# Optimization experiments

Measured on AMD Instinct MI355X. Metric: run time of the kernel, lower is better.

Reference implementation:

```python
import jax, jax.numpy as jnp
import numpy as np

B, INP, OUP = 16, 64, 64
T, H, W = 30, 64, 44
KD, KH, KW = 3, 3, 3
M, G = 2, 2
INP_GAP = max(16, INP // 16)          # 16
GROUPS = G * OUP                       # 128 (wn_fc2 groups)
IN_PG = (M * OUP) // GROUPS            # 1  in-channels per group
OUT_PG = (OUP * INP * KD * KH * KW) // GROUPS  # 864 out-channels per group


def setup_inputs() -> dict:
    key = jax.random.key(0)
    ks = jax.random.split(key, 6)
    x = jax.random.normal(ks[0], (B, INP, T, H, W), dtype=jnp.float32)
    # reduce: 1x1x1 conv INP -> INP_GAP (with bias), acts on [B, INP, 1,1,1]
    w_reduce = jax.random.normal(ks[1], (INP_GAP, INP), dtype=jnp.float32) * 0.05
    b_reduce = jax.random.normal(ks[2], (INP_GAP,), dtype=jnp.float32) * 0.05
    # wn_fc1: 1x1x1 conv INP_GAP -> M*OUP (with bias)
    w_fc1 = jax.random.normal(ks[3], (M * OUP, INP_GAP), dtype=jnp.float32) * 0.05
    b_fc1 = jax.random.normal(ks[4], (M * OUP,), dtype=jnp.float32) * 0.05
    # wn_fc2: grouped 1x1x1 conv, no bias: [groups, out_per_group, in_per_group]
    w_fc2 = jax.random.normal(ks[5], (GROUPS, OUT_PG, IN_PG), dtype=jnp.float32) * 0.02
    return {"x": x, "w_reduce": w_reduce, "b_reduce": b_reduce,
            "w_fc1": w_fc1, "b_fc1": b_fc1, "w_fc2": w_fc2}


def reference(x, w_reduce, b_reduce, w_fc1, b_fc1, w_fc2):
    # Global average pool over T,H,W -> [B, INP]; 1x1x1 convs are matmuls.
    x_gap = x.mean(axis=(2, 3, 4))                       # [B, INP]
    g = x_gap @ w_reduce.T + b_reduce                     # [B, INP_GAP]
    h = jax.nn.sigmoid(g @ w_fc1.T + b_fc1)               # [B, M*OUP]
    # Grouped 1x1 conv (groups=GROUPS): group-major channel layout matches
    # torch's conv output ordering, so a plain reshape reproduces .view().
    hg = h.reshape(B, GROUPS, IN_PG)                      # [B, G*OUP, 1]
    wdyn = jnp.einsum('goi,bgi->bgo', w_fc2, hg)          # [B, GROUPS, OUT_PG]
    wdyn = wdyn.reshape(B, OUP, INP, KD, KH, KW)          # per-sample conv weights

    # Per-sample conv3d (groups=1), stride 1, padding 1 on D,H,W.
    def conv_one(xi, wi):
        # xi: [INP, T, H, W], wi: [OUP, INP, KD, KH, KW]
        return jax.lax.conv_general_dilated(
            xi[None], wi, window_strides=(1, 1, 1),
            padding=[(1, 1), (1, 1), (1, 1)],
            dimension_numbers=('NCDHW', 'OIDHW', 'NCDHW'))[0]

    return jax.vmap(conv_one)(x, wdyn)                    # [B, OUP, T, H, W]
```

## Files before the change

kernel.cpp:

```cpp
#include <hip/hip_runtime.h>
#include <hip/hip_bf16.h>
#include <stdint.h>

#define B_ 16
#define T_ 30
#define H_ 64
#define W_ 44
#define HW_ (H_*W_)
#define THW_ (T_*HW_)

#define HP_ 66
#define WP_ 46
#define PPLANE_ (HP_*WP_)
#define PPOS_ (T_*PPLANE_)

#define TZ 4
#define TY 8
#define TX 16
#define SZ 6
#define SY 10
#define SX 18
#define NS (SZ*SY*SX)

typedef __bf16 bf16x8 __attribute__((ext_vector_type(8)));
typedef float f32x4 __attribute__((ext_vector_type(4)));

static __device__ __forceinline__ short f2bf(float f) {
    __hip_bfloat16 h = __float2bfloat16(f);
    union { __hip_bfloat16 b; short s; } u; u.b = h; return u.s;
}

static __device__ __forceinline__ void gload_lds16(const short* g, short* l) {
    __builtin_amdgcn_global_load_lds((const __attribute__((address_space(1))) void*)g,
                                     (__attribute__((address_space(3))) void*)l, 16, 0, 0);
}

__global__ __launch_bounds__(256) void transpose_kernel(const float* __restrict__ x,
                                                        short* __restrict__ xt) {
    __shared__ short lb[64*52];
    int blk = blockIdx.x;
    int b = blk / (T_*HP_);
    int r = blk - b*(T_*HP_);
    int t = r / HP_;
    int hp = r - t*HP_;
    int tid = threadIdx.x;
    bool interior = (hp >= 1) && (hp <= H_);
    if (interior) {
        int h = hp - 1;
        for (int e = tid; e < 704; e += 256) {
            int ic = e / 11, q = e - ic*11;
            const float4* p = (const float4*)(x + ((size_t)(b*64 + ic)*T_ + t)*HW_ + h*W_) + q;
            float4 v = *p;
            short4 s4;
            s4.x = f2bf(v.x); s4.y = f2bf(v.y); s4.z = f2bf(v.z); s4.w = f2bf(v.w);
            *(short4*)&lb[ic*52 + q*4] = s4;
        }
    }
    __syncthreads();
    for (int e = tid; e < WP_*16; e += 256) {
        int wp = e >> 4, i4 = (e & 15) * 4;
        short4 s4 = make_short4(0,0,0,0);
        if (interior && wp >= 1 && wp <= W_) {
            int w = wp - 1;
            s4.x = lb[(i4+0)*52 + w];
            s4.y = lb[(i4+1)*52 + w];
            s4.z = lb[(i4+2)*52 + w];
            s4.w = lb[(i4+3)*52 + w];
        }
        size_t pos = (size_t)t*PPLANE_ + hp*WP_ + wp;
        short* dst = xt + ((size_t)(b*2 + (i4 >> 5))*PPOS_ + pos)*32 + (i4 & 31);
        *(short4*)dst = s4;
    }
}

__global__ __launch_bounds__(256) void gap_kernel(const float* __restrict__ x,
                                                  float* __restrict__ gap) {
    int bc = blockIdx.x;
    const float4* p4 = (const float4*)(x + (size_t)bc * THW_);
    float sum = 0.f;
    for (int i = threadIdx.x; i < THW_ / 4; i += 256) {
        float4 v = p4[i];
        sum += (v.x + v.y) + (v.z + v.w);
    }
    #pragma unroll
    for (int o = 32; o > 0; o >>= 1) sum += __shfl_down(sum, o);
    __shared__ float partial[4];
    if ((threadIdx.x & 63) == 0) partial[threadIdx.x >> 6] = sum;
    __syncthreads();
    if (threadIdx.x == 0)
        gap[bc] = (partial[0] + partial[1] + partial[2] + partial[3]) * (1.0f / THW_);
}

__global__ __launch_bounds__(256) void fc_kernel(const float* __restrict__ gap,
        const float* __restrict__ w_reduce, const float* __restrict__ b_reduce,
        const float* __restrict__ w_fc1, const float* __restrict__ b_fc1,
        float* __restrict__ h_out) {
    __shared__ float gl[256];
    int t = threadIdx.x;
    {
        int b = t >> 4, j = t & 15;
        float a = b_reduce[j];
        #pragma unroll
        for (int c = 0; c < 64; ++c) a += gap[b*64 + c] * w_reduce[j*64 + c];
        gl[b*16 + j] = a;
    }
    __syncthreads();
    for (int idx = t; idx < 2048; idx += 256) {
        int b = idx >> 7, j = idx & 127;
        float v = b_fc1[j];
        #pragma unroll
        for (int i = 0; i < 16; ++i) v += gl[b*16 + i] * w_fc1[j*16 + i];
        h_out[idx] = 1.0f / (1.0f + expf(-v));
    }
}

__global__ __launch_bounds__(256) void wdyn_kernel(const float* __restrict__ w_fc2,
        const float* __restrict__ h, short* __restrict__ wdyn, short* __restrict__ zblk) {
    if (blockIdx.x == 0 && threadIdx.x < 128) zblk[threadIdx.x] = 0;
    int b = blockIdx.x / 27, tap = blockIdx.x % 27;
    short* dst = wdyn + ((size_t)b*27 + tap) * 4096;
    for (int e = threadIdx.x; e < 4096; e += 256) {
        int oc = e >> 6, ic = e & 63;
        float wv = w_fc2[(oc*64 + ic)*27 + tap];
        float hv = h[b*128 + 2*oc + (ic >> 5)];
        dst[e] = f2bf(wv * hv);
    }
}

__global__ __launch_bounds__(256, 2) void conv_kernel(const short* __restrict__ xt,
        const short* __restrict__ wdyn, const short* __restrict__ zblk,
        float* __restrict__ out) {
    __shared__ short xs[NS*32 + 256];
    __shared__ short wb[2][2048];

    int bid = blockIdx.x;
    int b = bid / 192; int r = bid - b*192;
    int tzt = r / 24; r -= tzt*24;
    int tyt = r / 3;  int txt = r - tyt*3;
    int t0 = tzt*TZ, h0 = tyt*TY, w0 = txt*TX;

    int tid = threadIdx.x, wid = tid >> 6, lane = tid & 63;
    int ln = lane & 15, kg = lane >> 4;
    int l4 = lane >> 2, c = lane & 3;

    const short* wdb = wdyn + (size_t)b * 27 * 4096;

    f32x4 acc[4][8];
    #pragma unroll
    for (int mt = 0; mt < 4; ++mt)
        #pragma unroll
        for (int j = 0; j < 8; ++j) acc[mt][j] = f32x4{0.f, 0.f, 0.f, 0.f};

    auto stage_w = [&](int step) {
        int tap = step % 27, half = step / 27;
        const short* base = wdb + tap*4096 + half*32;
        short* dst = wb[step & 1];
        #pragma unroll
        for (int jj = 0; jj < 4; ++jj) {
            int oc = jj*16 + l4;
            gload_lds16(base + oc*64 + ((c ^ (oc & 3)) * 8), dst + jj*512);
        }
    };
    auto stage_x = [&](int half) {
        const short* xbh = xt + (size_t)(b*2 + half) * PPOS_ * 32;
        #pragma unroll 2
        for (int ii = 0; ii < 17; ++ii) {
            int inst = wid*17 + ii;
            int s = inst*16 + l4;
            int z = s / 180; int rr = s - z*180;
            int y = rr / 18; int xx = rr - y*18;
            int t = t0 + z - 1;
            int seg = (c ^ (s & 3)) * 8;
            const short* src = ((unsigned)t < (unsigned)T_)
                ? xbh + ((size_t)t*PPLANE_ + (h0+y)*WP_ + (w0+xx))*32 + seg
                : zblk + seg;
            gload_lds16(src, xs + inst*512);
        }
    };

    stage_x(0);
    if (wid == 0) stage_w(0);
    __syncthreads();

    for (int step = 0; step < 54; ++step) {
        int nstep = step + 1;
        if (nstep < 54 && wid == (nstep & 3)) stage_w(nstep);

        int tap = step % 27;
        int kd = tap / 9; int rr = tap - kd*9; int kh = rr / 3; int kw = rr - kh*3;
        const short* wbp = wb[step & 1];
        bf16x8 a[4];
        #pragma unroll
        for (int mt = 0; mt < 4; ++mt) {
            int oc = mt*16 + ln;
            a[mt] = *(const bf16x8*)&wbp[oc*32 + ((kg ^ (oc & 3)) * 8)];
        }
        int sb = (wid + kd)*180 + kh*18 + kw + ln;
        #pragma unroll
        for (int j = 0; j < 8; ++j) {
            int s = sb + j*18;
            bf16x8 bv = *(const bf16x8*)&xs[s*32 + ((kg ^ (s & 3)) * 8)];
            acc[0][j] = __builtin_amdgcn_mfma_f32_16x16x32_bf16(a[0], bv, acc[0][j], 0, 0, 0);
            acc[1][j] = __builtin_amdgcn_mfma_f32_16x16x32_bf16(a[1], bv, acc[1][j], 0, 0, 0);
            acc[2][j] = __builtin_amdgcn_mfma_f32_16x16x32_bf16(a[2], bv, acc[2][j], 0, 0, 0);
            acc[3][j] = __builtin_amdgcn_mfma_f32_16x16x32_bf16(a[3], bv, acc[3][j], 0, 0, 0);
        }
        __syncthreads();
        if (step == 26) { stage_x(1); __syncthreads(); }
    }

    int t = t0 + wid;
    int wv = w0 + ln;
    if (t < T_ && wv < W_) {
        #pragma unroll
        for (int mt = 0; mt < 4; ++mt) {
            size_t obase = ((size_t)(b*64 + mt*16 + kg*4) * T_ + t) * HW_;
            #pragma unroll
            for (int j = 0; j < 8; ++j) {
                float* o = out + obase + (h0 + j)*W_ + wv;
                #pragma unroll
                for (int ri = 0; ri < 4; ++ri)
                    o[(size_t)ri * THW_] = acc[mt][j][ri];
            }
        }
    }
}

extern "C" void kernel_launch(void* const* d_in, const int* in_sizes, int n_in,
                              void* d_out, int out_size, void* d_ws, size_t ws_size,
                              hipStream_t stream) {
    const float* x        = (const float*)d_in[0];
    const float* w_reduce = (const float*)d_in[1];
    const float* b_reduce = (const float*)d_in[2];
    const float* w_fc1    = (const float*)d_in[3];
    const float* b_fc1    = (const float*)d_in[4];
    const float* w_fc2    = (const float*)d_in[5];
    float* out = (float*)d_out;

    float* gap  = (float*)d_ws;
    float* h    = gap + 1024;
    short* wdyn = (short*)(h + 2048);
    short* zblk = wdyn + (size_t)B_*27*4096;
    short* xt   = zblk + 128;

    transpose_kernel<<<B_*T_*HP_, 256, 0, stream>>>(x, xt);
    gap_kernel      <<<B_*64,     256, 0, stream>>>(x, gap);
    fc_kernel       <<<1,         256, 0, stream>>>(gap, w_reduce, b_reduce, w_fc1, b_fc1, h);
    wdyn_kernel     <<<B_*27,     256, 0, stream>>>(w_fc2, h, wdyn, zblk);
    conv_kernel     <<<B_*192,    256, 0, stream>>>(xt, wdyn, zblk, out);
}
```

Before: 607.2 us.

## Fuse GAP into transpose kernel and rework LDS swizzle and weight staging

Removes the separate global-average-pool kernel and computes per-channel sums inside the transpose kernel, using shared-memory atomics and then global atomics into a buffer zeroed by a memset. This saves a second full pass over x. It also pads the transpose LDS row stride from 52 to 53, changes the conv kernel's LDS XOR swizzle to use bits 1-2, and spreads weight staging across all four waves each step instead of one. The price is contention on the atomics and a summation order that is no longer deterministic.

```diff
diff --git a/kernel.cpp b/kernel.cpp
--- a/kernel.cpp
+++ b/kernel.cpp
@@ -22,6 +22,8 @@
 #define SX 18
 #define NS (SZ*SY*SX)
 
+#define SWZ(v) (((v) >> 1) & 3)
+
 typedef __bf16 bf16x8 __attribute__((ext_vector_type(8)));
 typedef float f32x4 __attribute__((ext_vector_type(4)));
 
@@ -36,14 +38,18 @@
 }
 
 __global__ __launch_bounds__(256) void transpose_kernel(const float* __restrict__ x,
-                                                        short* __restrict__ xt) {
-    __shared__ short lb[64*52];
+                                                        short* __restrict__ xt,
+                                                        float* __restrict__ gap) {
+    __shared__ short lb[64*53];
+    __shared__ float gsum[64];
     int blk = blockIdx.x;
     int b = blk / (T_*HP_);
     int r = blk - b*(T_*HP_);
     int t = r / HP_;
     int hp = r - t*HP_;
     int tid = threadIdx.x;
+    if (tid < 64) gsum[tid] = 0.f;
+    __syncthreads();
     bool interior = (hp >= 1) && (hp <= H_);
     if (interior) {
         int h = hp - 1;
@@ -53,42 +59,27 @@
             float4 v = *p;
             short4 s4;
             s4.x = f2bf(v.x); s4.y = f2bf(v.y); s4.z = f2bf(v.z); s4.w = f2bf(v.w);
-            *(short4*)&lb[ic*52 + q*4] = s4;
-        }
-    }
-    __syncthreads();
+            *(short4*)&lb[ic*53 + q*4] = s4;
+            atomicAdd(&gsum[ic], (v.x + v.y) + (v.z + v.w));
+        }
+    }
+    __syncthreads();
+    if (interior && tid < 64)
+        atomicAdd(&gap[b*64 + tid], gsum[tid] * (1.0f / THW_));
     for (int e = tid; e < WP_*16; e += 256) {
         int wp = e >> 4, i4 = (e & 15) * 4;
         short4 s4 = make_short4(0,0,0,0);
         if (interior && wp >= 1 && wp <= W_) {
             int w = wp - 1;
-            s4.x = lb[(i4+0)*52 + w];
-            s4.y = lb[(i4+1)*52 + w];
-            s4.z = lb[(i4+2)*52 + w];
-            s4.w = lb[(i4+3)*52 + w];
+            s4.x = lb[(i4+0)*53 + w];
+            s4.y = lb[(i4+1)*53 + w];
+            s4.z = lb[(i4+2)*53 + w];
+            s4.w = lb[(i4+3)*53 + w];
         }
         size_t pos = (size_t)t*PPLANE_ + hp*WP_ + wp;
         short* dst = xt + ((size_t)(b*2 + (i4 >> 5))*PPOS_ + pos)*32 + (i4 & 31);
         *(short4*)dst = s4;
     }
-}
-
-__global__ __launch_bounds__(256) void gap_kernel(const float* __restrict__ x,
-                                                  float* __restrict__ gap) {
-    int bc = blockIdx.x;
-    const float4* p4 = (const float4*)(x + (size_t)bc * THW_);
-    float sum = 0.f;
-    for (int i = threadIdx.x; i < THW_ / 4; i += 256) {
-        float4 v = p4[i];
-        sum += (v.x + v.y) + (v.z + v.w);
-    }
-    #pragma unroll
-    for (int o = 32; o > 0; o >>= 1) sum += __shfl_down(sum, o);
-    __shared__ float partial[4];
-    if ((threadIdx.x & 63) == 0) partial[threadIdx.x >> 6] = sum;
-    __syncthreads();
-    if (threadIdx.x == 0)
-        gap[bc] = (partial[0] + partial[1] + partial[2] + partial[3]) * (1.0f / THW_);
 }
 
 __global__ __launch_bounds__(256) void fc_kernel(const float* __restrict__ gap,
@@ -155,11 +146,8 @@
         int tap = step % 27, half = step / 27;
         const short* base = wdb + tap*4096 + half*32;
         short* dst = wb[step & 1];
-        #pragma unroll
-        for (int jj = 0; jj < 4; ++jj) {
-            int oc = jj*16 + l4;
-            gload_lds16(base + oc*64 + ((c ^ (oc & 3)) * 8), dst + jj*512);
-        }
+        int oc = wid*16 + l4;
+        gload_lds16(base + oc*64 + ((c ^ SWZ(oc)) * 8), dst + wid*512);
     };
     auto stage_x = [&](int half) {
         const short* xbh = xt + (size_t)(b*2 + half) * PPOS_ * 32;
@@ -170,7 +158,7 @@
             int z = s / 180; int rr = s - z*180;
             int y = rr / 18; int xx = rr - y*18;
             int t = t0 + z - 1;
-            int seg = (c ^ (s & 3)) * 8;
+            int seg = (c ^ SWZ(s)) * 8;
             const short* src = ((unsigned)t < (unsigned)T_)
                 ? xbh + ((size_t)t*PPLANE_ + (h0+y)*WP_ + (w0+xx))*32 + seg
                 : zblk + seg;
@@ -179,12 +167,12 @@
     };
 
     stage_x(0);
-    if (wid == 0) stage_w(0);
+    stage_w(0);
     __syncthreads();
 
     for (int step = 0; step < 54; ++step) {
         int nstep = step + 1;
-        if (nstep < 54 && wid == (nstep & 3)) stage_w(nstep);
+        if (nstep < 54) stage_w(nstep);
 
         int tap = step % 27;
         int kd = tap / 9; int rr = tap - kd*9; int kh = rr / 3; int kw = rr - kh*3;
@@ -193,13 +181,13 @@
         #pragma unroll
         for (int mt = 0; mt < 4; ++mt) {
             int oc = mt*16 + ln;
-            a[mt] = *(const bf16x8*)&wbp[oc*32 + ((kg ^ (oc & 3)) * 8)];
+            a[mt] = *(const bf16x8*)&wbp[oc*32 + ((kg ^ SWZ(oc)) * 8)];
         }
         int sb = (wid + kd)*180 + kh*18 + kw + ln;
         #pragma unroll
         for (int j = 0; j < 8; ++j) {
             int s = sb + j*18;
-            bf16x8 bv = *(const bf16x8*)&xs[s*32 + ((kg ^ (s & 3)) * 8)];
+            bf16x8 bv = *(const bf16x8*)&xs[s*32 + ((kg ^ SWZ(s)) * 8)];
             acc[0][j] = __builtin_amdgcn_mfma_f32_16x16x32_bf16(a[0], bv, acc[0][j], 0, 0, 0);
             acc[1][j] = __builtin_amdgcn_mfma_f32_16x16x32_bf16(a[1], bv, acc[1][j], 0, 0, 0);
             acc[2][j] = __builtin_amdgcn_mfma_f32_16x16x32_bf16(a[2], bv, acc[2][j], 0, 0, 0);
@@ -243,8 +231,8 @@
     short* zblk = wdyn + (size_t)B_*27*4096;
     short* xt   = zblk + 128;
 
-    transpose_kernel<<<B_*T_*HP_, 256, 0, stream>>>(x, xt);
-    gap_kernel      <<<B_*64,     256, 0, stream>>>(x, gap);
+    hipMemsetAsync(gap, 0, 1024*sizeof(float), stream);
+    transpose_kernel<<<B_*T_*HP_, 256, 0, stream>>>(x, xt, gap);
     fc_kernel       <<<1,         256, 0, stream>>>(gap, w_reduce, b_reduce, w_fc1, b_fc1, h);
     wdyn_kernel     <<<B_*27,     256, 0, stream>>>(w_fc2, h, wdyn, zblk);
     conv_kernel     <<<B_*192,    256, 0, stream>>>(xt, wdyn, zblk, out);
```

New measurement: 692.2 us. +14.0%, slower.
